# Performance work log

Hardware: AMD Instinct MI355X
Metric: run time of the kernel (lower is better)

## Reference

```python
import jax, jax.numpy as jnp
import numpy as np

B, N = 32, 512
N_DIM, N_P, N_K = 128, 3, 2
F0_DIM = N_DIM * N_P            # 384
CAT_DIM = N_DIM * (N_K + 1) * N_P  # 1152


def setup_inputs() -> dict:
    key = jax.random.key(0)
    ks = jax.random.split(key, 12)
    s = 0.05
    return {
        "loc": jax.random.uniform(ks[0], (B, N, 2), dtype=jnp.float32),
        "deadline": jax.random.uniform(ks[1], (B, N), dtype=jnp.float32),
        "workload": jax.random.uniform(ks[2], (B, N), dtype=jnp.float32),
        "depot": jax.random.uniform(ks[3], (B, 1, 2), dtype=jnp.float32),
        "W_init": jax.random.normal(ks[4], (3, F0_DIM), dtype=jnp.float32) * s,
        "b_init": jnp.zeros((F0_DIM,), jnp.float32),
        "W_dep": jax.random.normal(ks[5], (2, N_DIM), dtype=jnp.float32) * s,
        "b_dep": jnp.zeros((N_DIM,), jnp.float32),
        "W_g1": jax.random.normal(ks[6], (CAT_DIM, N_DIM), dtype=jnp.float32) * s,
        "b_g1": jnp.zeros((N_DIM,), jnp.float32),
        "W_g2": jax.random.normal(ks[7], (CAT_DIM, N_DIM), dtype=jnp.float32) * s,
        "b_g2": jnp.zeros((N_DIM,), jnp.float32),
        "W_g3": jax.random.normal(ks[8], (CAT_DIM, N_DIM), dtype=jnp.float32) * s,
        "b_g3": jnp.zeros((N_DIM,), jnp.float32),
        "gamma": jnp.ones((F0_DIM,), jnp.float32),
        "beta": jnp.zeros((F0_DIM,), jnp.float32),
        "W_F": jax.random.normal(ks[9], (F0_DIM, N_DIM), dtype=jnp.float32) * s,
        "b_F": jnp.zeros((N_DIM,), jnp.float32),
    }


def _forward(loc, deadline, workload, depot, W_init, b_init, W_dep, b_dep,
             W_g1, b_g1, W_g2, b_g2, W_g3, b_g3, gamma, beta, W_F, b_F):
    # X = [loc, deadline/deadline.max()] -> [B,N,3] (workload is concatenated then dropped in original)
    X = jnp.concatenate([loc, (deadline / deadline.max())[..., None]], axis=-1)
    n = X.shape[1]
    # pairwise squared distances [B,N,N]
    d2 = ((X[:, :, None, :] - X[:, None, :, :]) ** 2).sum(-1)
    off = ~jnp.eye(n, dtype=bool)                      # off-diagonal mask
    d2_safe = jnp.where(off, d2, 1.0)
    A = jnp.where(off, 1.0 / jnp.sqrt(d2_safe), 0.0)   # A = 1/dist off-diag, 0 on diag
    A = jnp.where(jnp.isnan(A), 0.0, A)                # A[A!=A]=0
    A = A / A.max()                                    # global max-normalize
    deg = A.sum(-1) - 1.0                              # (A.sum(-1) - 1)
    L = jnp.eye(n, dtype=A.dtype) * deg[:, None, :] - A  # D - A (diag = deg)
    L2 = L @ L

    F0 = X @ W_init + b_init                           # [B,N,384]
    F0_sq = F0 * F0
    F0_cu = F0 * F0_sq

    def prop(F):
        return jnp.concatenate([F, L @ F, L2 @ F], axis=-1)  # [B,N,1152]

    g1 = prop(F0) @ W_g1 + b_g1
    g2 = prop(F0_sq) @ W_g2 + b_g2
    g3 = prop(F0_cu) @ W_g3 + b_g3
    F1 = jnp.concatenate([g1, g2, g3], axis=-1)        # [B,N,384]
    F1 = jax.nn.leaky_relu(F1) + F0

    # BatchNorm1d (training mode): stats over flattened (B*N) samples, biased var
    flat = F1.reshape(-1, F1.shape[-1])
    mu = flat.mean(0)
    var = ((flat - mu) ** 2).mean(0)
    F1 = (F1 - mu) / jnp.sqrt(var + 1e-5) * gamma + beta

    F_final = jax.nn.leaky_relu(F1 @ W_F + b_F)        # [B,N,128]
    dep = depot @ W_dep + b_dep                        # [B,1,128]
    h = jnp.concatenate([dep, F_final], axis=1)        # [B,N+1,128]
    return h, h.mean(axis=1)


def reference(loc, deadline, workload, depot, W_init, b_init, W_dep, b_dep,
              W_g1, b_g1, W_g2, b_g2, W_g3, b_g3, gamma, beta, W_F, b_F):
    return _forward(loc, deadline, workload, depot, W_init, b_init, W_dep, b_dep,
                    W_g1, b_g1, W_g2, b_g2, W_g3, b_g3, gamma, beta, W_F, b_F)
```

## Files before the change

### kernel.cpp

```cpp
#include <hip/hip_runtime.h>

#define LEAKY(x) ((x) > 0.0f ? (x) : 0.01f * (x))

typedef __attribute__((ext_vector_type(8))) short bf16x8;
typedef __attribute__((ext_vector_type(4))) float f32x4;
typedef __attribute__((ext_vector_type(8))) unsigned short u16x8;
typedef __attribute__((ext_vector_type(4))) unsigned short u16x4;

__device__ __forceinline__ unsigned short f2bf(float f) {
    unsigned int u = __float_as_uint(f);
    unsigned int r = (u + 0x7fffu + ((u >> 16) & 1u)) >> 16;
    return (unsigned short)r;
}
__device__ __forceinline__ float bf2f(unsigned short u) {
    return __uint_as_float(((unsigned int)u) << 16);
}

__device__ __forceinline__ void lds_barrier() {
    __builtin_amdgcn_s_waitcnt(0xC07F);
    __builtin_amdgcn_s_barrier();
}


__global__ void k_dmax(const float* __restrict__ deadline, float* __restrict__ dmax) {
    __shared__ float red[256];
    int t = threadIdx.x;
    float m = -1e30f;
    for (int i = t; i < 16384; i += 256) m = fmaxf(m, deadline[i]);
    red[t] = m; __syncthreads();
    for (int s = 128; s > 0; s >>= 1) {
        if (t < s) red[t] = fmaxf(red[t], red[t + s]);
        __syncthreads();
    }
    if (t == 0) *dmax = red[0];
}

__global__ __launch_bounds__(256) void k_rowstats(const float* __restrict__ loc,
                                                  const float* __restrict__ deadline,
                                                  const float* __restrict__ dmaxv,
                                                  float* __restrict__ rowsum, float* __restrict__ pmax) {
    int blk = blockIdx.x;
    int wave = threadIdx.x >> 6, lane = threadIdx.x & 63;
    int bi = blk * 4 + wave;
    int b = bi >> 9, i = bi & 511;
    float invd = 1.0f / (*dmaxv);
    const float* lb = loc + b * 1024;
    const float* db = deadline + b * 512;
    float xi = lb[i * 2], yi = lb[i * 2 + 1], zi = db[i] * invd;
    float lsum = 0.f, lmax = 0.f;
    for (int j = lane; j < 512; j += 64) {
        float d0 = xi - lb[j * 2], d1 = yi - lb[j * 2 + 1], d2 = zi - db[j] * invd;
        float dd = d0 * d0 + d1 * d1 + d2 * d2;
        float r = (j == i) ? 0.f : rsqrtf(dd);
        lsum += r; lmax = fmaxf(lmax, r);
    }
    for (int off = 32; off > 0; off >>= 1) {
        lsum += __shfl_down(lsum, off);
        lmax = fmaxf(lmax, __shfl_down(lmax, off));
    }
    __shared__ float smax[4];
    if (lane == 0) { rowsum[bi] = lsum; smax[wave] = lmax; }
    __syncthreads();
    if (threadIdx.x == 0) pmax[blk] = fmaxf(fmaxf(smax[0], smax[1]), fmaxf(smax[2], smax[3]));
}

__global__ void k_amax(const float* __restrict__ pmax, float* __restrict__ amaxf) {
    __shared__ float red[256];
    int t = threadIdx.x;
    float m = 0.f;
    for (int i = t; i < 4096; i += 256) m = fmaxf(m, pmax[i]);
    red[t] = m; __syncthreads();
    for (int s = 128; s > 0; s >>= 1) {
        if (t < s) red[t] = fmaxf(red[t], red[t + s]);
        __syncthreads();
    }
    if (t == 0) *amaxf = red[0];
}

__global__ void k_buildL(const float* __restrict__ loc, const float* __restrict__ deadline,
                         const float* __restrict__ dmaxv, const float* __restrict__ rowsum,
                         const float* __restrict__ amaxf, unsigned short* __restrict__ Lb) {
    int id = blockIdx.x * 256 + threadIdx.x;
    float inv = 1.0f / (*amaxf);
    float invd = 1.0f / (*dmaxv);
    size_t e = (size_t)id * 4;
    size_t bi = e >> 9;
    int b = (int)(bi >> 9);
    int i = (int)(bi & 511);
    int j0 = (int)(e & 511);
    const float* lb = loc + b * 1024;
    const float* db = deadline + b * 512;
    float xi = lb[i * 2], yi = lb[i * 2 + 1], zi = db[i] * invd;
    float4 l01 = *(const float4*)(lb + j0 * 2);
    float4 l23 = *(const float4*)(lb + j0 * 2 + 4);
    float4 dj = *(const float4*)(db + j0);
    float diag = rowsum[bi] * inv - 1.0f;
    float jx[4] = {l01.x, l01.z, l23.x, l23.z};
    float jy[4] = {l01.y, l01.w, l23.y, l23.w};
    float jz[4] = {dj.x * invd, dj.y * invd, dj.z * invd, dj.w * invd};
    u16x4 o;
#pragma unroll
    for (int j = 0; j < 4; j++) {
        float d0 = xi - jx[j], d1 = yi - jy[j], d2 = zi - jz[j];
        float dd = d0 * d0 + d1 * d1 + d2 * d2;
        float v = (i == j0 + j) ? diag : -rsqrtf(dd) * inv;
        o[j] = f2bf(v);
    }
    *(u16x4*)(Lb + e) = o;
}

__global__ void k_F0pow(const float* __restrict__ loc, const float* __restrict__ deadline,
                        const float* __restrict__ dmaxv,
                        const float* __restrict__ Wi, const float* __restrict__ bi_,
                        unsigned short* __restrict__ P1, unsigned short* __restrict__ P2,
                        unsigned short* __restrict__ P3) {
    int id = blockIdx.x * 256 + threadIdx.x;
    int row = id / 96, c4 = (id % 96) * 4;
    float x0 = loc[row * 2], x1 = loc[row * 2 + 1], x2 = deadline[row] / (*dmaxv);
    float4 w0 = *(const float4*)(Wi + c4);
    float4 w1 = *(const float4*)(Wi + 384 + c4);
    float4 w2 = *(const float4*)(Wi + 768 + c4);
    float4 bb = *(const float4*)(bi_ + c4);
    float f[4] = {x0 * w0.x + x1 * w1.x + x2 * w2.x + bb.x,
                  x0 * w0.y + x1 * w1.y + x2 * w2.y + bb.y,
                  x0 * w0.z + x1 * w1.z + x2 * w2.z + bb.z,
                  x0 * w0.w + x1 * w1.w + x2 * w2.w + bb.w};
    u16x4 o1, o2, o3;
#pragma unroll
    for (int j = 0; j < 4; j++) {
        o1[j] = f2bf(f[j]); o2[j] = f2bf(f[j] * f[j]); o3[j] = f2bf(f[j] * f[j] * f[j]);
    }
    size_t e = (size_t)row * 384 + c4;
    *(u16x4*)(P1 + e) = o1; *(u16x4*)(P2 + e) = o2; *(u16x4*)(P3 + e) = o3;
}

__global__ void k_prepW(const float* __restrict__ Wg1, const float* __restrict__ Wg2,
                        const float* __restrict__ Wg3, unsigned short* __restrict__ WgT) {
    int id = blockIdx.x * 256 + threadIdx.x;
    int combo = id / 49152, rem = id % 49152;
    int n = rem / 384, k = rem % 384;
    int kp = combo / 3, part = combo % 3;
    const float* W = (kp == 0) ? Wg1 : (kp == 1 ? Wg2 : Wg3);
    WgT[id] = f2bf(W[(part * 384 + k) * 128 + n]);
}


__device__ __forceinline__ void pipe128x64(
    const unsigned short* __restrict__ A0, int As0, const unsigned short* __restrict__ B0, int Bs0, int it0,
    const unsigned short* __restrict__ A1, int As1, const unsigned short* __restrict__ B1, int Bs1, int it1,
    unsigned short* AsL, unsigned short* BsL,
    f32x4 (&acc)[4][2], int t)
{
    const int lane = t & 63, wave = t >> 6;
    const int wm = wave >> 1, wn = wave & 1;
    const int quad = lane >> 4, l16 = lane & 15;
    const int ra = t >> 1, ca = (t & 1) * 4;
    const int rb = t >> 2, cb = (t & 3) * 2;
    const unsigned short* Ar0 = A0 + (size_t)ra * As0;
    const unsigned short* Ar1 = A1 ? (A1 + (size_t)ra * As1) : Ar0;
    const unsigned short* Br0 = B0 + (size_t)rb * Bs0;
    const unsigned short* Br1 = B1 ? (B1 + (size_t)rb * Bs1) : Br0;
    const int total = it0 + it1;

    u16x8 paA[4], pbA[2], paB[4], pbB[2];

    auto loadStage = [&](int idx, u16x8 (&pa)[4], u16x8 (&pb)[2]) {
        int sg = (idx >= it0);
        int k0 = (sg ? idx - it0 : idx) * 64;
        const unsigned short* Ar = sg ? Ar1 : Ar0;
        const unsigned short* Br = sg ? Br1 : Br0;
#pragma unroll
        for (int j = 0; j < 4; j++) pa[j] = *(const u16x8*)(Ar + k0 + (ca + j) * 8);
#pragma unroll
        for (int j = 0; j < 2; j++) pb[j] = *(const u16x8*)(Br + k0 + (cb + j) * 8);
    };
    auto writeStage = [&](int bf_, u16x8 (&pa)[4], u16x8 (&pb)[2]) {
#pragma unroll
        for (int j = 0; j < 4; j++)
            *(u16x8*)(AsL + bf_ * 8192 + ra * 64 + (((ca + j) ^ (ra & 7)) * 8)) = pa[j];
#pragma unroll
        for (int j = 0; j < 2; j++)
            *(u16x8*)(BsL + bf_ * 4096 + rb * 64 + (((cb + j) ^ (rb & 7)) * 8)) = pb[j];
    };
    auto mfmaStep = [&](int bf_) {
#pragma unroll
        for (int h = 0; h < 2; h++) {
            bf16x8 af[4], bfr[2];
            int phys = ((h * 4 + quad) ^ (l16 & 7)) * 8;
#pragma unroll
            for (int i = 0; i < 4; i++)
                af[i] = *(const bf16x8*)(AsL + bf_ * 8192 + (wm * 64 + i * 16 + l16) * 64 + phys);
#pragma unroll
            for (int n = 0; n < 2; n++)
                bfr[n] = *(const bf16x8*)(BsL + bf_ * 4096 + (wn * 32 + n * 16 + l16) * 64 + phys);
#pragma unroll
            for (int i = 0; i < 4; i++)
#pragma unroll
                for (int n = 0; n < 2; n++)
                    acc[i][n] = __builtin_amdgcn_mfma_f32_16x16x32_bf16(af[i], bfr[n], acc[i][n], 0, 0, 0);
        }
    };

    loadStage(0, paA, pbA);
    loadStage(1, paB, pbB);

    int buf = 0;
    for (int s = 0; s < total; s += 2) {
        writeStage(buf, paA, pbA);
        lds_barrier();
        if (s + 2 < total) loadStage(s + 2, paA, pbA);
        mfmaStep(buf);
        buf ^= 1;

        writeStage(buf, paB, pbB);
        lds_barrier();
        if (s + 3 < total) loadStage(s + 3, paB, pbB);
        mfmaStep(buf);
        buf ^= 1;
    }
}

__device__ __forceinline__ void pipe64x64(
    const unsigned short* __restrict__ A0, int As0, const unsigned short* __restrict__ B0, int Bs0, int it0,
    unsigned short* AsL, unsigned short* BsL,
    f32x4 (&acc)[2][2], int t)
{
    const int lane = t & 63, wave = t >> 6;
    const int wm = wave >> 1, wn = wave & 1;
    const int quad = lane >> 4, l16 = lane & 15;
    const int rb = t >> 2, cb = (t & 3) * 2;
    const unsigned short* Ar0 = A0 + (size_t)rb * As0;
    const unsigned short* Br0 = B0 + (size_t)rb * Bs0;

    u16x8 paA[2], pbA[2], paB[2], pbB[2];
    auto loadStage = [&](int idx, u16x8 (&pa)[2], u16x8 (&pb)[2]) {
        int k0 = idx * 64;
#pragma unroll
        for (int j = 0; j < 2; j++) { pa[j] = *(const u16x8*)(Ar0 + k0 + (cb + j) * 8);
                                      pb[j] = *(const u16x8*)(Br0 + k0 + (cb + j) * 8); }
    };
    auto writeStage = [&](int bf_, u16x8 (&pa)[2], u16x8 (&pb)[2]) {
#pragma unroll
        for (int j = 0; j < 2; j++) {
            int phys = ((cb + j) ^ (rb & 7)) * 8;
            *(u16x8*)(AsL + bf_ * 4096 + rb * 64 + phys) = pa[j];
            *(u16x8*)(BsL + bf_ * 4096 + rb * 64 + phys) = pb[j];
        }
    };
    auto mfmaStep = [&](int bf_) {
#pragma unroll
        for (int h = 0; h < 2; h++) {
            bf16x8 af[2], bfr[2];
            int phys = ((h * 4 + quad) ^ (l16 & 7)) * 8;
#pragma unroll
            for (int i = 0; i < 2; i++)
                af[i] = *(const bf16x8*)(AsL + bf_ * 4096 + (wm * 32 + i * 16 + l16) * 64 + phys);
#pragma unroll
            for (int n = 0; n < 2; n++)
                bfr[n] = *(const bf16x8*)(BsL + bf_ * 4096 + (wn * 32 + n * 16 + l16) * 64 + phys);
#pragma unroll
            for (int i = 0; i < 2; i++)
#pragma unroll
                for (int n = 0; n < 2; n++)
                    acc[i][n] = __builtin_amdgcn_mfma_f32_16x16x32_bf16(af[i], bfr[n], acc[i][n], 0, 0, 0);
        }
    };

    loadStage(0, paA, pbA);
    loadStage(1, paB, pbB);
    int buf = 0;
    for (int s = 0; s < it0; s += 2) {
        writeStage(buf, paA, pbA);
        lds_barrier();
        if (s + 2 < it0) loadStage(s + 2, paA, pbA);
        mfmaStep(buf);
        buf ^= 1;
        writeStage(buf, paB, pbB);
        lds_barrier();
        if (s + 3 < it0) loadStage(s + 3, paB, pbB);
        mfmaStep(buf);
        buf ^= 1;
    }
}

__global__ __launch_bounds__(256) void k_ygemmT(
    const unsigned short* __restrict__ WgT,
    const unsigned short* __restrict__ P1, const unsigned short* __restrict__ P2,
    const unsigned short* __restrict__ P3, unsigned short* __restrict__ Y2T)
{
    __shared__ unsigned short AsL[16384], BsL[8192];
    const int t = threadIdx.x;
    const int id = blockIdx.x;
    const int b = id & 31, tt = id >> 5;
    const int kp = tt % 3, nb = tt / 3;
    const unsigned short* P = (kp == 0) ? P1 : (kp == 1 ? P2 : P3);
    f32x4 acc[4][2];
#pragma unroll
    for (int i = 0; i < 4; i++)
#pragma unroll
        for (int n = 0; n < 2; n++) acc[i][n] = (f32x4){0.f, 0.f, 0.f, 0.f};
    pipe128x64(WgT + (size_t)(kp * 3 + 2) * 49152, 384,
               P + ((size_t)b * 512 + nb * 64) * 384, 384, 6,
               nullptr, 0, nullptr, 0, 0, AsL, BsL, acc, t);

    const int wave = t >> 6, lane = t & 63;
    const int wm = wave >> 1, wn = wave & 1;
    const int quad = lane >> 4, l16 = lane & 15;
#pragma unroll
    for (int i = 0; i < 4; i++)
#pragma unroll
        for (int n = 0; n < 2; n++) {
            int g = kp * 128 + wm * 64 + i * 16 + quad * 4;
            int node = nb * 64 + wn * 32 + n * 16 + l16;
#pragma unroll
            for (int r = 0; r < 4; r++)
                Y2T[((size_t)b * 384 + g + r) * 512 + node] = f2bf(acc[i][n][r]);
        }
}

__global__ __launch_bounds__(256) void k_lg1T(
    const unsigned short* __restrict__ Lb, const unsigned short* __restrict__ Y2T,
    const unsigned short* __restrict__ WgT,
    const unsigned short* __restrict__ P1, const unsigned short* __restrict__ P2,
    const unsigned short* __restrict__ P3, unsigned short* __restrict__ ZT)
{
    __shared__ unsigned short AsL[16384], BsL[8192];
    const int t = threadIdx.x;
    const int id = blockIdx.x;
    const int b = id & 31, tt = id >> 5;
    const int kp = tt % 3, nb = tt / 3;
    const unsigned short* P = (kp == 0) ? P1 : (kp == 1 ? P2 : P3);
    f32x4 acc[4][2];
#pragma unroll
    for (int i = 0; i < 4; i++)
#pragma unroll
        for (int n = 0; n < 2; n++) acc[i][n] = (f32x4){0.f, 0.f, 0.f, 0.f};
    pipe128x64(Y2T + (size_t)b * 196608 + (size_t)kp * 128 * 512, 512,
               Lb + (size_t)b * 262144 + (size_t)nb * 64 * 512, 512, 8,
               WgT + (size_t)(kp * 3 + 1) * 49152, 384,
               P + ((size_t)b * 512 + nb * 64) * 384, 384, 6, AsL, BsL, acc, t);

    const int wave = t >> 6, lane = t & 63;
    const int wm = wave >> 1, wn = wave & 1;
    const int quad = lane >> 4, l16 = lane & 15;
#pragma unroll
    for (int i = 0; i < 4; i++)
#pragma unroll
        for (int n = 0; n < 2; n++) {
            int g = kp * 128 + wm * 64 + i * 16 + quad * 4;
            int node = nb * 64 + wn * 32 + n * 16 + l16;
#pragma unroll
            for (int r = 0; r < 4; r++)
                ZT[((size_t)b * 384 + g + r) * 512 + node] = f2bf(acc[i][n][r]);
        }
}

__global__ __launch_bounds__(256) void k_lg2(
    const unsigned short* __restrict__ Lb, const unsigned short* __restrict__ ZT,
    const unsigned short* __restrict__ WgT,
    const unsigned short* __restrict__ P1, const unsigned short* __restrict__ P2,
    const unsigned short* __restrict__ P3,
    const float* __restrict__ bg1, const float* __restrict__ bg2, const float* __restrict__ bg3,
    unsigned short* __restrict__ F1b, float* __restrict__ bn1, float* __restrict__ bn2)
{
    __shared__ unsigned short AsL[16384], BsL[8192];
    __shared__ float bnS[64], bnQ[64];
    const int t = threadIdx.x;
    const int id = blockIdx.x;
    const int b = id & 31, tt = id >> 5;
    const int gt = tt % 6, mb = tt / 6;
    const int kp = gt >> 1;
    if (t < 64) { bnS[t] = 0.f; bnQ[t] = 0.f; }
    const unsigned short* P = (kp == 0) ? P1 : (kp == 1 ? P2 : P3);
    f32x4 acc[4][2];
#pragma unroll
    for (int i = 0; i < 4; i++)
#pragma unroll
        for (int n = 0; n < 2; n++) acc[i][n] = (f32x4){0.f, 0.f, 0.f, 0.f};
    pipe128x64(Lb + (size_t)b * 262144 + (size_t)mb * 128 * 512, 512,
               ZT + (size_t)b * 196608 + (size_t)gt * 64 * 512, 512, 8,
               P + ((size_t)b * 512 + mb * 128) * 384, 384,
               WgT + (size_t)(kp * 3) * 49152 + (size_t)(gt & 1) * 64 * 384, 384, 6,
               AsL, BsL, acc, t);

    const int wave = t >> 6, lane = t & 63;
    const int wm = wave >> 1, wn = wave & 1;
    const int quad = lane >> 4, l16 = lane & 15;
    const float* bg = (kp == 0) ? bg1 : (kp == 1 ? bg2 : bg3);
    float ls1[2], ls2[2];
#pragma unroll
    for (int n = 0; n < 2; n++) { ls1[n] = 0.f; ls2[n] = 0.f; }
#pragma unroll
    for (int i = 0; i < 4; i++) {
        int rowl = mb * 128 + wm * 64 + i * 16 + quad * 4;
        size_t rowg = (size_t)b * 512 + rowl;
#pragma unroll
        for (int n = 0; n < 2; n++) {
            int nloc = wn * 32 + n * 16 + l16;
            int g = gt * 64 + nloc;
            float bias = bg[(gt & 1) * 64 + nloc];
#pragma unroll
            for (int r = 0; r < 4; r++) {
                size_t idx = (rowg + r) * 384 + g;
                float c = acc[i][n][r] + bias;
                float v = LEAKY(c) + bf2f(P1[idx]);
                F1b[idx] = f2bf(v);
                ls1[n] += v; ls2[n] += v * v;
            }
        }
    }
#pragma unroll
    for (int n = 0; n < 2; n++) {
        int nloc = wn * 32 + n * 16 + l16;
        atomicAdd(&bnS[nloc], ls1[n]);
        atomicAdd(&bnQ[nloc], ls2[n]);
    }
    __syncthreads();
    if (t < 64) {
        atomicAdd(&bn1[gt * 64 + t], bnS[t]);
        atomicAdd(&bn2[gt * 64 + t], bnQ[t]);
    }
}

__global__ __launch_bounds__(384) void k_bnfin_beff(
    const float* __restrict__ bn1, const float* __restrict__ bn2,
    const float* __restrict__ gamma, const float* __restrict__ beta,
    const float* __restrict__ WF, const float* __restrict__ bF,
    float* __restrict__ sS, float* __restrict__ beffv)
{
    __shared__ float ttL[384];
    int c = threadIdx.x;
    float mu = bn1[c] * (1.f / 16384.f);
    float var = bn2[c] * (1.f / 16384.f) - mu * mu;
    float sc = gamma[c] / sqrtf(var + 1e-5f);
    sS[c] = sc;
    ttL[c] = beta[c] - mu * sc;
    __syncthreads();
    if (c < 128) {
        float a = bF[c];
        for (int k = 0; k < 384; k++) a += ttL[k] * WF[k * 128 + c];
        beffv[c] = a;
    }
}

__global__ void k_fold(const float* __restrict__ WF, const float* __restrict__ sS,
                       unsigned short* __restrict__ WFsT) {
    int id = blockIdx.x * 256 + threadIdx.x;
    int n = id / 384, k = id % 384;
    WFsT[id] = f2bf(WF[k * 128 + n] * sS[k]);
}

__global__ __launch_bounds__(256) void k_fgemm(
    const unsigned short* __restrict__ F1b, const unsigned short* __restrict__ WFsT,
    const float* __restrict__ beffv, float* __restrict__ out, float* __restrict__ msum)
{
    __shared__ unsigned short AsL[8192], BsL[8192];
    __shared__ float msS[64];
    const int t = threadIdx.x;
    const int id = blockIdx.x;
    const int b = id & 31, tt = id >> 5;
    const int seg = tt >> 1, nt = tt & 1;
    if (t < 64) msS[t] = 0.f;
    f32x4 acc[2][2];
#pragma unroll
    for (int i = 0; i < 2; i++)
#pragma unroll
        for (int n = 0; n < 2; n++) acc[i][n] = (f32x4){0.f, 0.f, 0.f, 0.f};
    pipe64x64(F1b + ((size_t)b * 512 + seg * 64) * 384, 384,
              WFsT + (size_t)nt * 64 * 384, 384, 6, AsL, BsL, acc, t);

    const int wave = t >> 6, lane = t & 63;
    const int wm = wave >> 1, wn = wave & 1;
    const int quad = lane >> 4, l16 = lane & 15;
    float ls[2];
#pragma unroll
    for (int n = 0; n < 2; n++) ls[n] = 0.f;
#pragma unroll
    for (int i = 0; i < 2; i++) {
        int nd = seg * 64 + wm * 32 + i * 16 + quad * 4;
#pragma unroll
        for (int n = 0; n < 2; n++) {
            int col = nt * 64 + wn * 32 + n * 16 + l16;
            float bb = beffv[col];
#pragma unroll
            for (int r = 0; r < 4; r++) {
                float x = acc[i][n][r] + bb;
                float v = LEAKY(x);
                out[(size_t)b * 65664 + (size_t)(nd + r + 1) * 128 + col] = v;
                ls[n] += v;
            }
        }
    }
#pragma unroll
    for (int n = 0; n < 2; n++) atomicAdd(&msS[wn * 32 + n * 16 + l16], ls[n]);
    __syncthreads();
    if (t < 64) atomicAdd(&msum[b * 128 + nt * 64 + t], msS[t]);
}

__global__ void k_meandep(const float* __restrict__ depot, const float* __restrict__ Wd,
                          const float* __restrict__ bd, const float* __restrict__ msum,
                          float* __restrict__ out) {
    int id = blockIdx.x * 256 + threadIdx.x;
    int b = id >> 7, o = id & 127;
    float dep = depot[b * 2] * Wd[o] + depot[b * 2 + 1] * Wd[128 + o] + bd[o];
    out[(size_t)b * 65664 + o] = dep;
    out[2101248 + id] = (msum[id] + dep) * (1.0f / 513.0f);
}


extern "C" void kernel_launch(void* const* d_in, const int* in_sizes, int n_in,
                              void* d_out, int out_size, void* d_ws, size_t ws_size,
                              hipStream_t stream) {
    const float* loc      = (const float*)d_in[0];
    const float* deadline = (const float*)d_in[1];
    const float* depot    = (const float*)d_in[3];
    const float* W_init   = (const float*)d_in[4];
    const float* b_init   = (const float*)d_in[5];
    const float* W_dep    = (const float*)d_in[6];
    const float* b_dep    = (const float*)d_in[7];
    const float* W_g1     = (const float*)d_in[8];
    const float* b_g1     = (const float*)d_in[9];
    const float* W_g2     = (const float*)d_in[10];
    const float* b_g2     = (const float*)d_in[11];
    const float* W_g3     = (const float*)d_in[12];
    const float* b_g3     = (const float*)d_in[13];
    const float* gamma    = (const float*)d_in[14];
    const float* beta     = (const float*)d_in[15];
    const float* W_F      = (const float*)d_in[16];
    const float* b_F      = (const float*)d_in[17];
    float* out = (float*)d_out;
    float* ws  = (float*)d_ws;

    float* dmaxv  = ws + 0;
    float* amaxf  = ws + 4;
    float* bn1    = ws + 8;
    float* bn2    = ws + 392;
    float* msum   = ws + 776;
    float* rowsum = ws + 4872;
    float* pmax   = ws + 21256;
    float* sS     = ws + 25352;
    float* beffv  = ws + 25736;
    unsigned short* Lb   = (unsigned short*)(ws + 25864);
    unsigned short* P1   = (unsigned short*)(ws + 4220168);
    unsigned short* P2   = (unsigned short*)(ws + 7365896);
    unsigned short* P3   = (unsigned short*)(ws + 10511624);
    unsigned short* WgT  = (unsigned short*)(ws + 13657352);
    unsigned short* WFsT = (unsigned short*)(ws + 13878536);
    unsigned short* Y2T  = (unsigned short*)(ws + 13903112);
    unsigned short* ZT   = (unsigned short*)(ws + 17048840);
    unsigned short* F1b  = (unsigned short*)(ws + 20194568);

    hipMemsetAsync(bn1, 0, (384 + 384 + 4096) * sizeof(float), stream);

    k_dmax<<<1, 256, 0, stream>>>(deadline, dmaxv);
    k_rowstats<<<4096, 256, 0, stream>>>(loc, deadline, dmaxv, rowsum, pmax);
    k_amax<<<1, 256, 0, stream>>>(pmax, amaxf);
    k_buildL<<<8192, 256, 0, stream>>>(loc, deadline, dmaxv, rowsum, amaxf, Lb);
    k_F0pow<<<6144, 256, 0, stream>>>(loc, deadline, dmaxv, W_init, b_init, P1, P2, P3);
    k_prepW<<<1728, 256, 0, stream>>>(W_g1, W_g2, W_g3, WgT);

    k_ygemmT<<<768, 256, 0, stream>>>(WgT, P1, P2, P3, Y2T);
    k_lg1T<<<768, 256, 0, stream>>>(Lb, Y2T, WgT, P1, P2, P3, ZT);
    k_lg2<<<768, 256, 0, stream>>>(Lb, ZT, WgT, P1, P2, P3,
                                   b_g1, b_g2, b_g3, F1b, bn1, bn2);

    k_bnfin_beff<<<1, 384, 0, stream>>>(bn1, bn2, gamma, beta, W_F, b_F, sS, beffv);
    k_fold<<<192, 256, 0, stream>>>(W_F, sS, WFsT);
    k_fgemm<<<512, 256, 0, stream>>>(F1b, WFsT, beffv, out, msum);
    k_meandep<<<16, 256, 0, stream>>>(depot, W_dep, b_dep, msum, out);
}
```

Measured before the change: 240.0 us.

## Stage GEMM epilogues through LDS for coalesced stores and merge small kernels

GEMM epilogues in ygemmT, lg1T, lg2 and fgemm now write accumulators to shared memory first, then issue vectorized row-contiguous global stores. Previously each lane scattered 2-byte or 4-byte writes at large strides. Small prep kernels are also merged: F0pow with prepW, and BN finalize with the weight fold and depot embedding. This cuts launch count and serialization. The costs are extra LDS traffic and barriers, plus redundant BN-scale recomputation per element in the fold.

```diff
diff --git a/kernel.cpp b/kernel.cpp
--- a/kernel.cpp
+++ b/kernel.cpp
@@ -109,39 +109,41 @@
     *(u16x4*)(Lb + e) = o;
 }
 
-__global__ void k_F0pow(const float* __restrict__ loc, const float* __restrict__ deadline,
-                        const float* __restrict__ dmaxv,
-                        const float* __restrict__ Wi, const float* __restrict__ bi_,
-                        unsigned short* __restrict__ P1, unsigned short* __restrict__ P2,
-                        unsigned short* __restrict__ P3) {
-    int id = blockIdx.x * 256 + threadIdx.x;
-    int row = id / 96, c4 = (id % 96) * 4;
-    float x0 = loc[row * 2], x1 = loc[row * 2 + 1], x2 = deadline[row] / (*dmaxv);
-    float4 w0 = *(const float4*)(Wi + c4);
-    float4 w1 = *(const float4*)(Wi + 384 + c4);
-    float4 w2 = *(const float4*)(Wi + 768 + c4);
-    float4 bb = *(const float4*)(bi_ + c4);
-    float f[4] = {x0 * w0.x + x1 * w1.x + x2 * w2.x + bb.x,
-                  x0 * w0.y + x1 * w1.y + x2 * w2.y + bb.y,
-                  x0 * w0.z + x1 * w1.z + x2 * w2.z + bb.z,
-                  x0 * w0.w + x1 * w1.w + x2 * w2.w + bb.w};
-    u16x4 o1, o2, o3;
-#pragma unroll
-    for (int j = 0; j < 4; j++) {
-        o1[j] = f2bf(f[j]); o2[j] = f2bf(f[j] * f[j]); o3[j] = f2bf(f[j] * f[j] * f[j]);
-    }
-    size_t e = (size_t)row * 384 + c4;
-    *(u16x4*)(P1 + e) = o1; *(u16x4*)(P2 + e) = o2; *(u16x4*)(P3 + e) = o3;
-}
-
-__global__ void k_prepW(const float* __restrict__ Wg1, const float* __restrict__ Wg2,
-                        const float* __restrict__ Wg3, unsigned short* __restrict__ WgT) {
-    int id = blockIdx.x * 256 + threadIdx.x;
-    int combo = id / 49152, rem = id % 49152;
-    int n = rem / 384, k = rem % 384;
-    int kp = combo / 3, part = combo % 3;
-    const float* W = (kp == 0) ? Wg1 : (kp == 1 ? Wg2 : Wg3);
-    WgT[id] = f2bf(W[(part * 384 + k) * 128 + n]);
+__global__ void k_F0powW(const float* __restrict__ loc, const float* __restrict__ deadline,
+                         const float* __restrict__ dmaxv,
+                         const float* __restrict__ Wi, const float* __restrict__ bi_,
+                         const float* __restrict__ Wg1, const float* __restrict__ Wg2,
+                         const float* __restrict__ Wg3,
+                         unsigned short* __restrict__ P1, unsigned short* __restrict__ P2,
+                         unsigned short* __restrict__ P3, unsigned short* __restrict__ WgT) {
+    int bid = blockIdx.x;
+    if (bid < 6144) {
+        int id = bid * 256 + threadIdx.x;
+        int row = id / 96, c4 = (id % 96) * 4;
+        float x0 = loc[row * 2], x1 = loc[row * 2 + 1], x2 = deadline[row] / (*dmaxv);
+        float4 w0 = *(const float4*)(Wi + c4);
+        float4 w1 = *(const float4*)(Wi + 384 + c4);
+        float4 w2 = *(const float4*)(Wi + 768 + c4);
+        float4 bb = *(const float4*)(bi_ + c4);
+        float f[4] = {x0 * w0.x + x1 * w1.x + x2 * w2.x + bb.x,
+                      x0 * w0.y + x1 * w1.y + x2 * w2.y + bb.y,
+                      x0 * w0.z + x1 * w1.z + x2 * w2.z + bb.z,
+                      x0 * w0.w + x1 * w1.w + x2 * w2.w + bb.w};
+        u16x4 o1, o2, o3;
+#pragma unroll
+        for (int j = 0; j < 4; j++) {
+            o1[j] = f2bf(f[j]); o2[j] = f2bf(f[j] * f[j]); o3[j] = f2bf(f[j] * f[j] * f[j]);
+        }
+        size_t e = (size_t)row * 384 + c4;
+        *(u16x4*)(P1 + e) = o1; *(u16x4*)(P2 + e) = o2; *(u16x4*)(P3 + e) = o3;
+    } else {
+        int id = (bid - 6144) * 256 + threadIdx.x;
+        int combo = id / 49152, rem = id % 49152;
+        int n = rem / 384, k = rem % 384;
+        int kp = combo / 3, part = combo % 3;
+        const float* W = (kp == 0) ? Wg1 : (kp == 1 ? Wg2 : Wg3);
+        WgT[id] = f2bf(W[(part * 384 + k) * 128 + n]);
+    }
 }
 
 
@@ -163,7 +165,6 @@
     const int total = it0 + it1;
 
     u16x8 paA[4], pbA[2], paB[4], pbB[2];
-
     auto loadStage = [&](int idx, u16x8 (&pa)[4], u16x8 (&pb)[2]) {
         int sg = (idx >= it0);
         int k0 = (sg ? idx - it0 : idx) * 64;
@@ -203,7 +204,6 @@
 
     loadStage(0, paA, pbA);
     loadStage(1, paB, pbB);
-
     int buf = 0;
     for (int s = 0; s < total; s += 2) {
         writeStage(buf, paA, pbA);
@@ -211,7 +211,6 @@
         if (s + 2 < total) loadStage(s + 2, paA, pbA);
         mfmaStep(buf);
         buf ^= 1;
-
         writeStage(buf, paB, pbB);
         lds_barrier();
         if (s + 3 < total) loadStage(s + 3, paB, pbB);
@@ -283,12 +282,37 @@
     }
 }
 
+__device__ __forceinline__ void storeCT_bf16(
+    f32x4 (&acc)[4][2], unsigned short* LDSu, int t, unsigned short* __restrict__ dst)
+{
+    const int wave = t >> 6, lane = t & 63;
+    const int wm = wave >> 1, wn = wave & 1;
+    const int quad = lane >> 4, l16 = lane & 15;
+    __syncthreads();
+    unsigned short* Cs = LDSu;
+#pragma unroll
+    for (int i = 0; i < 4; i++)
+#pragma unroll
+        for (int n = 0; n < 2; n++)
+#pragma unroll
+            for (int r = 0; r < 4; r++)
+                Cs[(wm * 64 + i * 16 + quad * 4 + r) * 72 + wn * 32 + n * 16 + l16] = f2bf(acc[i][n][r]);
+    __syncthreads();
+#pragma unroll
+    for (int v = 0; v < 4; v++) {
+        int chunk = t + v * 256;
+        int row = chunk >> 3, c8 = (chunk & 7) * 8;
+        u16x8 val = *(u16x8*)(Cs + row * 72 + c8);
+        *(u16x8*)(dst + (size_t)row * 512 + c8) = val;
+    }
+}
+
 __global__ __launch_bounds__(256) void k_ygemmT(
     const unsigned short* __restrict__ WgT,
     const unsigned short* __restrict__ P1, const unsigned short* __restrict__ P2,
     const unsigned short* __restrict__ P3, unsigned short* __restrict__ Y2T)
 {
-    __shared__ unsigned short AsL[16384], BsL[8192];
+    __shared__ unsigned short LDSu[24576];
     const int t = threadIdx.x;
     const int id = blockIdx.x;
     const int b = id & 31, tt = id >> 5;
@@ -301,21 +325,8 @@
         for (int n = 0; n < 2; n++) acc[i][n] = (f32x4){0.f, 0.f, 0.f, 0.f};
     pipe128x64(WgT + (size_t)(kp * 3 + 2) * 49152, 384,
                P + ((size_t)b * 512 + nb * 64) * 384, 384, 6,
-               nullptr, 0, nullptr, 0, 0, AsL, BsL, acc, t);
-
-    const int wave = t >> 6, lane = t & 63;
-    const int wm = wave >> 1, wn = wave & 1;
-    const int quad = lane >> 4, l16 = lane & 15;
-#pragma unroll
-    for (int i = 0; i < 4; i++)
-#pragma unroll
-        for (int n = 0; n < 2; n++) {
-            int g = kp * 128 + wm * 64 + i * 16 + quad * 4;
-            int node = nb * 64 + wn * 32 + n * 16 + l16;
-#pragma unroll
-            for (int r = 0; r < 4; r++)
-                Y2T[((size_t)b * 384 + g + r) * 512 + node] = f2bf(acc[i][n][r]);
-        }
+               nullptr, 0, nullptr, 0, 0, LDSu, LDSu + 16384, acc, t);
+    storeCT_bf16(acc, LDSu, t, Y2T + ((size_t)b * 384 + kp * 128) * 512 + nb * 64);
 }
 
 __global__ __launch_bounds__(256) void k_lg1T(
@@ -324,7 +335,7 @@
     const unsigned short* __restrict__ P1, const unsigned short* __restrict__ P2,
     const unsigned short* __restrict__ P3, unsigned short* __restrict__ ZT)
 {
-    __shared__ unsigned short AsL[16384], BsL[8192];
+    __shared__ unsigned short LDSu[24576];
     const int t = threadIdx.x;
     const int id = blockIdx.x;
     const int b = id & 31, tt = id >> 5;
@@ -338,21 +349,8 @@
     pipe128x64(Y2T + (size_t)b * 196608 + (size_t)kp * 128 * 512, 512,
                Lb + (size_t)b * 262144 + (size_t)nb * 64 * 512, 512, 8,
                WgT + (size_t)(kp * 3 + 1) * 49152, 384,
-               P + ((size_t)b * 512 + nb * 64) * 384, 384, 6, AsL, BsL, acc, t);
-
-    const int wave = t >> 6, lane = t & 63;
-    const int wm = wave >> 1, wn = wave & 1;
-    const int quad = lane >> 4, l16 = lane & 15;
-#pragma unroll
-    for (int i = 0; i < 4; i++)
-#pragma unroll
-        for (int n = 0; n < 2; n++) {
-            int g = kp * 128 + wm * 64 + i * 16 + quad * 4;
-            int node = nb * 64 + wn * 32 + n * 16 + l16;
-#pragma unroll
-            for (int r = 0; r < 4; r++)
-                ZT[((size_t)b * 384 + g + r) * 512 + node] = f2bf(acc[i][n][r]);
-        }
+               P + ((size_t)b * 512 + nb * 64) * 384, 384, 6, LDSu, LDSu + 16384, acc, t);
+    storeCT_bf16(acc, LDSu, t, ZT + ((size_t)b * 384 + kp * 128) * 512 + nb * 64);
 }
 
 __global__ __launch_bounds__(256) void k_lg2(
@@ -363,7 +361,7 @@
     const float* __restrict__ bg1, const float* __restrict__ bg2, const float* __restrict__ bg3,
     unsigned short* __restrict__ F1b, float* __restrict__ bn1, float* __restrict__ bn2)
 {
-    __shared__ unsigned short AsL[16384], BsL[8192];
+    __shared__ unsigned short LDSu[24576];
     __shared__ float bnS[64], bnQ[64];
     const int t = threadIdx.x;
     const int id = blockIdx.x;
@@ -381,39 +379,49 @@
                ZT + (size_t)b * 196608 + (size_t)gt * 64 * 512, 512, 8,
                P + ((size_t)b * 512 + mb * 128) * 384, 384,
                WgT + (size_t)(kp * 3) * 49152 + (size_t)(gt & 1) * 64 * 384, 384, 6,
-               AsL, BsL, acc, t);
+               LDSu, LDSu + 16384, acc, t);
 
     const int wave = t >> 6, lane = t & 63;
     const int wm = wave >> 1, wn = wave & 1;
     const int quad = lane >> 4, l16 = lane & 15;
+    __syncthreads();
+    float* Cf = (float*)LDSu;
+#pragma unroll
+    for (int i = 0; i < 4; i++)
+#pragma unroll
+        for (int n = 0; n < 2; n++)
+#pragma unroll
+            for (int r = 0; r < 4; r++)
+                Cf[(wm * 64 + i * 16 + quad * 4 + r) * 68 + wn * 32 + n * 16 + l16] = acc[i][n][r];
+    __syncthreads();
+
     const float* bg = (kp == 0) ? bg1 : (kp == 1 ? bg2 : bg3);
-    float ls1[2], ls2[2];
-#pragma unroll
-    for (int n = 0; n < 2; n++) { ls1[n] = 0.f; ls2[n] = 0.f; }
-#pragma unroll
-    for (int i = 0; i < 4; i++) {
-        int rowl = mb * 128 + wm * 64 + i * 16 + quad * 4;
-        size_t rowg = (size_t)b * 512 + rowl;
-#pragma unroll
-        for (int n = 0; n < 2; n++) {
-            int nloc = wn * 32 + n * 16 + l16;
-            int g = gt * 64 + nloc;
-            float bias = bg[(gt & 1) * 64 + nloc];
-#pragma unroll
-            for (int r = 0; r < 4; r++) {
-                size_t idx = (rowg + r) * 384 + g;
-                float c = acc[i][n][r] + bias;
-                float v = LEAKY(c) + bf2f(P1[idx]);
-                F1b[idx] = f2bf(v);
-                ls1[n] += v; ls2[n] += v * v;
-            }
+    float4 bgv = *(const float4*)(bg + (gt & 1) * 64 + (t & 15) * 4);
+    float ls1[4] = {0.f, 0.f, 0.f, 0.f}, ls2[4] = {0.f, 0.f, 0.f, 0.f};
+#pragma unroll
+    for (int v = 0; v < 8; v++) {
+        int chunk = t + v * 256;
+        int row = chunk >> 4;
+        int c4 = (chunk & 15) * 4;
+        float4 a = *(float4*)(Cf + row * 68 + c4);
+        size_t idx = ((size_t)b * 512 + mb * 128 + row) * 384 + gt * 64 + c4;
+        u16x4 p = *(const u16x4*)(P1 + idx);
+        float av[4] = {a.x, a.y, a.z, a.w};
+        float bv[4] = {bgv.x, bgv.y, bgv.z, bgv.w};
+        u16x4 o;
+#pragma unroll
+        for (int j = 0; j < 4; j++) {
+            float c = av[j] + bv[j];
+            float vv = LEAKY(c) + bf2f(p[j]);
+            o[j] = f2bf(vv);
+            ls1[j] += vv; ls2[j] += vv * vv;
         }
-    }
-#pragma unroll
-    for (int n = 0; n < 2; n++) {
-        int nloc = wn * 32 + n * 16 + l16;
-        atomicAdd(&bnS[nloc], ls1[n]);
-        atomicAdd(&bnQ[nloc], ls2[n]);
+        *(u16x4*)(F1b + idx) = o;
+    }
+#pragma unroll
+    for (int j = 0; j < 4; j++) {
+        atomicAdd(&bnS[(t & 15) * 4 + j], ls1[j]);
+        atomicAdd(&bnQ[(t & 15) * 4 + j], ls2[j]);
     }
     __syncthreads();
     if (t < 64) {
@@ -422,39 +430,44 @@
     }
 }
 
-__global__ __launch_bounds__(384) void k_bnfin_beff(
-    const float* __restrict__ bn1, const float* __restrict__ bn2,
-    const float* __restrict__ gamma, const float* __restrict__ beta,
-    const float* __restrict__ WF, const float* __restrict__ bF,
-    float* __restrict__ sS, float* __restrict__ beffv)
-{
-    __shared__ float ttL[384];
-    int c = threadIdx.x;
-    float mu = bn1[c] * (1.f / 16384.f);
-    float var = bn2[c] * (1.f / 16384.f) - mu * mu;
-    float sc = gamma[c] / sqrtf(var + 1e-5f);
-    sS[c] = sc;
-    ttL[c] = beta[c] - mu * sc;
-    __syncthreads();
-    if (c < 128) {
-        float a = bF[c];
-        for (int k = 0; k < 384; k++) a += ttL[k] * WF[k * 128 + c];
-        beffv[c] = a;
-    }
-}
-
-__global__ void k_fold(const float* __restrict__ WF, const float* __restrict__ sS,
-                       unsigned short* __restrict__ WFsT) {
-    int id = blockIdx.x * 256 + threadIdx.x;
-    int n = id / 384, k = id % 384;
-    WFsT[id] = f2bf(WF[k * 128 + n] * sS[k]);
+__global__ void k_bnfold(const float* __restrict__ bn1, const float* __restrict__ bn2,
+                         const float* __restrict__ gamma, const float* __restrict__ beta,
+                         const float* __restrict__ WF, const float* __restrict__ bF,
+                         const float* __restrict__ depot, const float* __restrict__ Wd,
+                         const float* __restrict__ bd,
+                         unsigned short* __restrict__ WFsT, float* __restrict__ beffv,
+                         float* __restrict__ out) {
+    int bid = blockIdx.x, t = threadIdx.x;
+    if (bid < 192) {
+        int id = bid * 256 + t;
+        int n = id / 384, k = id % 384;
+        float mu = bn1[k] * (1.f / 16384.f);
+        float var = bn2[k] * (1.f / 16384.f) - mu * mu;
+        float sc = gamma[k] / sqrtf(var + 1e-5f);
+        WFsT[id] = f2bf(WF[k * 128 + n] * sc);
+    } else if (bid == 192) {
+        if (t < 128) {
+            float a = bF[t];
+            for (int k = 0; k < 384; k++) {
+                float mu = bn1[k] * (1.f / 16384.f);
+                float var = bn2[k] * (1.f / 16384.f) - mu * mu;
+                float sc = gamma[k] / sqrtf(var + 1e-5f);
+                a += (beta[k] - mu * sc) * WF[k * 128 + t];
+            }
+            beffv[t] = a;
+        }
+    } else {
+        int id = (bid - 193) * 256 + t;
+        int b = id >> 7, o = id & 127;
+        out[(size_t)b * 65664 + o] = depot[b * 2] * Wd[o] + depot[b * 2 + 1] * Wd[128 + o] + bd[o];
+    }
 }
 
 __global__ __launch_bounds__(256) void k_fgemm(
     const unsigned short* __restrict__ F1b, const unsigned short* __restrict__ WFsT,
     const float* __restrict__ beffv, float* __restrict__ out, float* __restrict__ msum)
 {
-    __shared__ unsigned short AsL[8192], BsL[8192];
+    __shared__ unsigned short LDSu[16384];
     __shared__ float msS[64];
     const int t = threadIdx.x;
     const int id = blockIdx.x;
@@ -467,43 +480,50 @@
 #pragma unroll
         for (int n = 0; n < 2; n++) acc[i][n] = (f32x4){0.f, 0.f, 0.f, 0.f};
     pipe64x64(F1b + ((size_t)b * 512 + seg * 64) * 384, 384,
-              WFsT + (size_t)nt * 64 * 384, 384, 6, AsL, BsL, acc, t);
+              WFsT + (size_t)nt * 64 * 384, 384, 6, LDSu, LDSu + 8192, acc, t);
 
     const int wave = t >> 6, lane = t & 63;
     const int wm = wave >> 1, wn = wave & 1;
     const int quad = lane >> 4, l16 = lane & 15;
-    float ls[2];
-#pragma unroll
-    for (int n = 0; n < 2; n++) ls[n] = 0.f;
-#pragma unroll
-    for (int i = 0; i < 2; i++) {
-        int nd = seg * 64 + wm * 32 + i * 16 + quad * 4;
-#pragma unroll
-        for (int n = 0; n < 2; n++) {
-            int col = nt * 64 + wn * 32 + n * 16 + l16;
-            float bb = beffv[col];
-#pragma unroll
-            for (int r = 0; r < 4; r++) {
-                float x = acc[i][n][r] + bb;
-                float v = LEAKY(x);
-                out[(size_t)b * 65664 + (size_t)(nd + r + 1) * 128 + col] = v;
-                ls[n] += v;
-            }
-        }
-    }
-#pragma unroll
-    for (int n = 0; n < 2; n++) atomicAdd(&msS[wn * 32 + n * 16 + l16], ls[n]);
+    __syncthreads();
+    float* Cf = (float*)LDSu;
+#pragma unroll
+    for (int i = 0; i < 2; i++)
+#pragma unroll
+        for (int n = 0; n < 2; n++)
+#pragma unroll
+            for (int r = 0; r < 4; r++)
+                Cf[(wm * 32 + i * 16 + quad * 4 + r) * 68 + wn * 32 + n * 16 + l16] = acc[i][n][r];
+    __syncthreads();
+
+    float4 be = *(const float4*)(beffv + nt * 64 + (t & 15) * 4);
+    float ls[4] = {0.f, 0.f, 0.f, 0.f};
+#pragma unroll
+    for (int v = 0; v < 4; v++) {
+        int chunk = t + v * 256;
+        int row = chunk >> 4;
+        int c4 = (chunk & 15) * 4;
+        float4 a = *(float4*)(Cf + row * 68 + c4);
+        float av[4] = {a.x, a.y, a.z, a.w};
+        float bv[4] = {be.x, be.y, be.z, be.w};
+        float4 o;
+        float vv0 = LEAKY(av[0] + bv[0]); ls[0] += vv0;
+        float vv1 = LEAKY(av[1] + bv[1]); ls[1] += vv1;
+        float vv2 = LEAKY(av[2] + bv[2]); ls[2] += vv2;
+        float vv3 = LEAKY(av[3] + bv[3]); ls[3] += vv3;
+        o = make_float4(vv0, vv1, vv2, vv3);
+        *(float4*)(out + (size_t)b * 65664 + (size_t)(seg * 64 + row + 1) * 128 + nt * 64 + c4) = o;
+    }
+#pragma unroll
+    for (int j = 0; j < 4; j++) atomicAdd(&msS[(t & 15) * 4 + j], ls[j]);
     __syncthreads();
     if (t < 64) atomicAdd(&msum[b * 128 + nt * 64 + t], msS[t]);
 }
 
-__global__ void k_meandep(const float* __restrict__ depot, const float* __restrict__ Wd,
-                          const float* __restrict__ bd, const float* __restrict__ msum,
-                          float* __restrict__ out) {
+__global__ void k_mean(const float* __restrict__ msum, float* __restrict__ out) {
     int id = blockIdx.x * 256 + threadIdx.x;
     int b = id >> 7, o = id & 127;
-    float dep = depot[b * 2] * Wd[o] + depot[b * 2 + 1] * Wd[128 + o] + bd[o];
-    out[(size_t)b * 65664 + o] = dep;
+    float dep = out[(size_t)b * 65664 + o];
     out[2101248 + id] = (msum[id] + dep) * (1.0f / 513.0f);
 }
 
@@ -538,7 +558,6 @@
     float* msum   = ws + 776;
     float* rowsum = ws + 4872;
     float* pmax   = ws + 21256;
-    float* sS     = ws + 25352;
     float* beffv  = ws + 25736;
     unsigned short* Lb   = (unsigned short*)(ws + 25864);
     unsigned short* P1   = (unsigned short*)(ws + 4220168);
@@ -556,16 +575,16 @@
     k_rowstats<<<4096, 256, 0, stream>>>(loc, deadline, dmaxv, rowsum, pmax);
     k_amax<<<1, 256, 0, stream>>>(pmax, amaxf);
     k_buildL<<<8192, 256, 0, stream>>>(loc, deadline, dmaxv, rowsum, amaxf, Lb);
-    k_F0pow<<<6144, 256, 0, stream>>>(loc, deadline, dmaxv, W_init, b_init, P1, P2, P3);
-    k_prepW<<<1728, 256, 0, stream>>>(W_g1, W_g2, W_g3, WgT);
+    k_F0powW<<<7872, 256, 0, stream>>>(loc, deadline, dmaxv, W_init, b_init,
+                                       W_g1, W_g2, W_g3, P1, P2, P3, WgT);
 
     k_ygemmT<<<768, 256, 0, stream>>>(WgT, P1, P2, P3, Y2T);
     k_lg1T<<<768, 256, 0, stream>>>(Lb, Y2T, WgT, P1, P2, P3, ZT);
     k_lg2<<<768, 256, 0, stream>>>(Lb, ZT, WgT, P1, P2, P3,
                                    b_g1, b_g2, b_g3, F1b, bn1, bn2);
 
-    k_bnfin_beff<<<1, 384, 0, stream>>>(bn1, bn2, gamma, beta, W_F, b_F, sS, beffv);
-    k_fold<<<192, 256, 0, stream>>>(W_F, sS, WFsT);
+    k_bnfold<<<209, 256, 0, stream>>>(bn1, bn2, gamma, beta, W_F, b_F,
+                                      depot, W_dep, b_dep, WFsT, beffv, out);
     k_fgemm<<<512, 256, 0, stream>>>(F1b, WFsT, beffv, out, msum);
-    k_meandep<<<16, 256, 0, stream>>>(depot, W_dep, b_dep, msum, out);
-}
+    k_mean<<<16, 256, 0, stream>>>(msum, out);
+}
```

After: 271.0 us. 1.13x slower.
